# Kernel tuning notes

Hardware: AMD Instinct MI355X
Metric: run time of the kernel (lower is better)

The kernel has to match this reference:

```python
import jax, jax.numpy as jnp
import numpy as np

B, LQ, LK, D = 8, 2048, 2048, 128

def setup_inputs() -> dict:
    key = jax.random.key(0)
    k1, k2, k3, k4 = jax.random.split(key, 4)
    return {
        "query": jax.random.normal(k1, (B, LQ, D), dtype=jnp.float32),
        "key": jax.random.normal(k2, (B, LK, D), dtype=jnp.float32),
        "value": jax.random.normal(k3, (B, LK, D), dtype=jnp.float32),
        "scale_factor": jax.random.normal(k4, (B, LQ, LK), dtype=jnp.float32),
    }

def reference(query, key, value, scale_factor):
    # qk: [B, LQ, LK]
    qk = jnp.einsum("bqd,bkd->bqk", query, key)
    probs = jax.nn.softmax(qk * scale_factor, axis=-1)
    # dropout_p = 0.0 -> identity
    return jnp.einsum("bqk,bkd->bqd", probs, value)
```

## Files before the change

kernel.cpp:

```cpp
#include <hip/hip_runtime.h>
#include <hip/hip_bf16.h>


typedef float          f32x4  __attribute__((ext_vector_type(4)));
typedef float          f32x16 __attribute__((ext_vector_type(16)));
typedef short          s16x8  __attribute__((ext_vector_type(8)));
typedef unsigned int   u32x4  __attribute__((ext_vector_type(4)));
typedef unsigned short u16x4  __attribute__((ext_vector_type(4)));

typedef const __attribute__((address_space(1))) unsigned int* gas_ptr;
typedef __attribute__((address_space(3))) unsigned int*       las_ptr;

#define LOG2E 1.4426950408889634f

__device__ __forceinline__ float fast_exp2(float x) {
#if __has_builtin(__builtin_amdgcn_exp2f)
    return __builtin_amdgcn_exp2f(x);
#else
    return exp2f(x);
#endif
}
__device__ __forceinline__ unsigned short f2bf(float x) {
    return __builtin_bit_cast(unsigned short, __float2bfloat16(x));
}
__device__ __forceinline__ float bf2f(unsigned short u) {
    return __bfloat162float(__builtin_bit_cast(__hip_bfloat16, u));
}

__global__ void conv_split2(const float* __restrict__ q, const float* __restrict__ k,
                            unsigned short* __restrict__ qh, unsigned short* __restrict__ ql,
                            unsigned short* __restrict__ kh, unsigned short* __restrict__ kl) {
    const int bid  = blockIdx.x;
    const int half = bid >> 11;
    const int i    = (bid & 2047) * 256 + threadIdx.x;
    const float* src = half ? k : q;
    unsigned short* hi = half ? kh : qh;
    unsigned short* lo = half ? kl : ql;
    const float4 v = ((const float4*)src)[i];
    float f[4] = {v.x, v.y, v.z, v.w};
    u16x4 h, l;
#pragma unroll
    for (int j = 0; j < 4; ++j) {
        unsigned short hb = f2bf(f[j]);
        h[j] = hb;
        l[j] = f2bf(f[j] - bf2f(hb));
    }
    ((u16x4*)hi)[i] = h;
    ((u16x4*)lo)[i] = l;
}

__global__ void transpose_v(const float* __restrict__ v,
                            unsigned short* __restrict__ vt) {
    __shared__ unsigned short tile[64 * 36];
    const int b    = blockIdx.x & 7;
    const int rest = blockIdx.x >> 3;
    const int k0   = (rest & 31) * 64;
    const int d0   = (rest >> 5) * 32;
    const int tid  = threadIdx.x;
#pragma unroll
    for (int it = 0; it < 2; ++it) {
        int idx = it * 256 + tid;
        int kk  = idx >> 3;
        int d4  = idx & 7;
        float4 val = ((const float4*)v)[((b * 2048 + k0 + kk) * 128 + d0 + d4 * 4) >> 2];
        u16x4 t4;
        t4[0] = f2bf(val.x); t4[1] = f2bf(val.y);
        t4[2] = f2bf(val.z); t4[3] = f2bf(val.w);
        *(u16x4*)&tile[kk * 36 + d4 * 4] = t4;
    }
    __syncthreads();
    {
        int d  = tid >> 3;
        int k8 = tid & 7;
        u16x4 a, cgrp;
#pragma unroll
        for (int j = 0; j < 4; ++j) a[j]    = tile[(k8 * 8 + j) * 36 + d];
#pragma unroll
        for (int j = 0; j < 4; ++j) cgrp[j] = tile[(k8 * 8 + 4 + j) * 36 + d];
        unsigned short* outp = vt + (b * 128 + d0 + d) * 2048 + k0 + k8 * 8;
        *(u16x4*)outp       = a;
        *(u16x4*)(outp + 4) = cgrp;
    }
}

#define NKC 16
#define LDS_TOTAL 79360
#define PBUF_OFF  67584
#define MSTAT_OFF 77824
#define LSTAT_OFF 78848

__global__ __launch_bounds__(256, 2)
void flash_fwd(const unsigned short* __restrict__ qh_g,
               const unsigned short* __restrict__ ql_g,
               const unsigned short* __restrict__ kh_g,
               const unsigned short* __restrict__ kl_g,
               const unsigned short* __restrict__ vt_g,
               const float* __restrict__ scale_g,
               float* __restrict__ out) {
    __shared__ unsigned char smem[LDS_TOTAL];
    unsigned char* khbuf = smem;
    float* mstat = (float*)(smem + MSTAT_OFF);
    float* lstat = (float*)(smem + LSTAT_OFF);
    float* oex   = (float*)smem;

    const int tid  = threadIdx.x;
    const int wave = tid >> 6;
    const int lane = tid & 63;
    const int qi   = lane & 31;
    const int g2   = lane >> 5;

    const int bid = blockIdx.x;
    const int b   = bid & 7;
    const int qt  = bid >> 3;
    const int q0  = qt * 32;
    const int qrow = b * 2048 + q0 + qi;

    unsigned short* pw = (unsigned short*)(smem + PBUF_OFF + wave * 2560);

    s16x8 qhB[8], qlB[8];
#pragma unroll
    for (int s = 0; s < 8; ++s) {
        int idx = qrow * 16 + s * 2 + g2;
        qhB[s] = __builtin_bit_cast(s16x8, ((const u32x4*)qh_g)[idx]);
        qlB[s] = __builtin_bit_cast(s16x8, ((const u32x4*)ql_g)[idx]);
    }

    f32x16 oacc[4];
#pragma unroll
    for (int t = 0; t < 4; ++t)
#pragma unroll
        for (int r = 0; r < 16; ++r) oacc[t][r] = 0.f;
    float m_run = -INFINITY, l_run = 0.f;

    const int krow_base = b * 2048;

    {
#pragma unroll
        for (int j = 0; j < 8; ++j) {
            int o  = wave * 8192 + j * 1024 + lane * 16;
            int r  = o >> 8;
            int cp = (o >> 4) & 15;
            int cn = cp ^ (r & 7);
            const unsigned short* src = kh_g + ((krow_base + r) * 16 + cn) * 8;
            __builtin_amdgcn_global_load_lds((gas_ptr)(const void*)src,
                (las_ptr)(void*)(khbuf + wave * 8192 + j * 1024), 16, 0, 0);
        }
    }
    f32x4 scf[4];
    {
        const int sidx = qrow * 512 + wave * 8 + g2;
#pragma unroll
        for (int rg = 0; rg < 4; ++rg)
            scf[rg] = ((const f32x4*)scale_g)[sidx + rg * 2];
    }
    __syncthreads();

    for (int kc = 0; kc < NKC; ++kc) {
        const int k0  = kc * 128;
        const int cur = kc & 1;
        unsigned char* bufc = khbuf + cur * 32768;

        if (kc + 1 < NKC) {
            unsigned char* bufn = khbuf + (cur ^ 1) * 32768;
#pragma unroll
            for (int j = 0; j < 8; ++j) {
                int o  = wave * 8192 + j * 1024 + lane * 16;
                int r  = o >> 8;
                int cp = (o >> 4) & 15;
                int cn = cp ^ (r & 7);
                const unsigned short* src = kh_g + ((krow_base + k0 + 128 + r) * 16 + cn) * 8;
                __builtin_amdgcn_global_load_lds((gas_ptr)(const void*)src,
                    (las_ptr)(void*)(bufn + wave * 8192 + j * 1024), 16, 0, 0);
            }
        }

        u32x4 klr[8], vr[8];
        {
            const int krow = krow_base + k0 + wave * 32 + qi;
#pragma unroll
            for (int s = 0; s < 8; ++s)
                klr[s] = ((const u32x4*)kl_g)[krow * 16 + s * 2 + g2];
            const int vbase = (b * 128 + qi) * 256 + ((k0 + wave * 32) >> 3) + g2;
#pragma unroll
            for (int t = 0; t < 4; ++t)
#pragma unroll
                for (int s2 = 0; s2 < 2; ++s2)
                    vr[t * 2 + s2] = ((const u32x4*)vt_g)[vbase + t * 32 * 256 + s2 * 2];
        }

        f32x4 scn[4];
        if (kc + 1 < NKC) {
            const int sidx = qrow * 512 + ((k0 + 128) >> 2) + wave * 8 + g2;
#pragma unroll
            for (int rg = 0; rg < 4; ++rg)
                scn[rg] = ((const f32x4*)scale_g)[sidx + rg * 2];
        }

        f32x16 S;
#pragma unroll
        for (int r = 0; r < 16; ++r) S[r] = 0.f;
        s16x8 khf[8];
        {
            const int r  = wave * 32 + qi;
            const int rx = r & 7;
#pragma unroll
            for (int s = 0; s < 8; ++s) {
                int cp = (s * 2 + g2) ^ rx;
                khf[s] = *(const s16x8*)(bufc + r * 256 + cp * 16);
                S = __builtin_amdgcn_mfma_f32_32x32x16_bf16(khf[s], qhB[s], S, 0, 0, 0);
            }
#pragma unroll
            for (int s = 0; s < 8; ++s)
                S = __builtin_amdgcn_mfma_f32_32x32x16_bf16(
                        __builtin_bit_cast(s16x8, klr[s]), qhB[s], S, 0, 0, 0);
#pragma unroll
            for (int s = 0; s < 8; ++s)
                S = __builtin_amdgcn_mfma_f32_32x32x16_bf16(khf[s], qlB[s], S, 0, 0, 0);
        }

        float lt[16];
        float mx = -INFINITY;
#pragma unroll
        for (int r = 0; r < 16; ++r) {
            lt[r] = S[r] * (scf[r >> 2][r & 3] * LOG2E);
            mx = fmaxf(mx, lt[r]);
        }
        mx = fmaxf(mx, __shfl_xor(mx, 32));
        const int par = (kc & 1) * 128;
        if (g2 == 0) mstat[par + wave * 32 + qi] = mx;
        __syncthreads();

        float m_new = m_run;
#pragma unroll
        for (int w = 0; w < 4; ++w)
            m_new = fmaxf(m_new, mstat[par + w * 32 + qi]);
        const float al = fast_exp2(m_run - m_new);
        m_run = m_new;
#pragma unroll
        for (int t = 0; t < 4; ++t)
#pragma unroll
            for (int r = 0; r < 16; ++r) oacc[t][r] *= al;

        float rs = 0.f;
#pragma unroll
        for (int p = 0; p < 8; ++p) {
            float e0 = fast_exp2(lt[2 * p]     - m_new);
            float e1 = fast_exp2(lt[2 * p + 1] - m_new);
            rs += e0 + e1;
            unsigned int pk = (unsigned int)f2bf(e0) | ((unsigned int)f2bf(e1) << 16);
            int kk0 = ((2 * p) & 3) + 8 * (p >> 1) + 4 * g2;
            *(unsigned int*)&pw[qi * 40 + kk0] = pk;
        }
        rs += __shfl_xor(rs, 32);
        l_run = l_run * al + rs;

        s16x8 bP[2];
#pragma unroll
        for (int s2 = 0; s2 < 2; ++s2)
            bP[s2] = *(const s16x8*)&pw[qi * 40 + s2 * 16 + g2 * 8];
#pragma unroll
        for (int t = 0; t < 4; ++t)
#pragma unroll
            for (int s2 = 0; s2 < 2; ++s2)
                oacc[t] = __builtin_amdgcn_mfma_f32_32x32x16_bf16(
                            __builtin_bit_cast(s16x8, vr[t * 2 + s2]), bP[s2], oacc[t], 0, 0, 0);

        if (kc + 1 < NKC) {
#pragma unroll
            for (int rg = 0; rg < 4; ++rg) scf[rg] = scn[rg];
        }
    }

    if (g2 == 0) lstat[wave * 32 + qi] = l_run;
#pragma unroll
    for (int t = 0; t < 4; ++t)
#pragma unroll
        for (int rg = 0; rg < 4; ++rg) {
            f32x4 v4;
#pragma unroll
            for (int j = 0; j < 4; ++j) v4[j] = oacc[t][rg * 4 + j];
            *(f32x4*)&oex[(wave * 32 + qi) * 132 + t * 32 + rg * 8 + g2 * 4] = v4;
        }
    __syncthreads();
    {
        const int q    = tid >> 3;
        const int dblk = tid & 7;
        const float linv = 1.f / (lstat[q] + lstat[32 + q] + lstat[64 + q] + lstat[96 + q]);
#pragma unroll
        for (int j = 0; j < 4; ++j) {
            const int d = dblk * 16 + j * 4;
            f32x4 acc = *(const f32x4*)&oex[q * 132 + d];
#pragma unroll
            for (int w = 1; w < 4; ++w) {
                f32x4 p = *(const f32x4*)&oex[(w * 32 + q) * 132 + d];
                acc[0] += p[0]; acc[1] += p[1]; acc[2] += p[2]; acc[3] += p[3];
            }
            acc[0] *= linv; acc[1] *= linv; acc[2] *= linv; acc[3] *= linv;
            *(f32x4*)&out[(size_t)(b * 2048 + q0 + q) * 128 + d] = acc;
        }
    }
}

extern "C" void kernel_launch(void* const* d_in, const int* in_sizes, int n_in,
                              void* d_out, int out_size, void* d_ws, size_t ws_size,
                              hipStream_t stream) {
    const float* q  = (const float*)d_in[0];
    const float* k  = (const float*)d_in[1];
    const float* v  = (const float*)d_in[2];
    const float* sc = (const float*)d_in[3];
    float* out = (float*)d_out;

    char* ws = (char*)d_ws;
    const size_t MB = 1024 * 1024;
    unsigned short* qh = (unsigned short*)(ws);
    unsigned short* ql = (unsigned short*)(ws + 4 * MB);
    unsigned short* kh = (unsigned short*)(ws + 8 * MB);
    unsigned short* kl = (unsigned short*)(ws + 12 * MB);
    unsigned short* vt = (unsigned short*)(ws + 16 * MB);

    conv_split2<<<4096, 256, 0, stream>>>(q, k, qh, ql, kh, kl);
    transpose_v<<<1024, 256, 0, stream>>>(v, vt);
    flash_fwd<<<512, 256, 0, stream>>>(qh, ql, kh, kl, vt, sc, out);
}
```

Baseline: 299.7 us.

## Rewrite attention with fp16 split, fragment-major layouts, single-wave blocks

Replaces the bf16 hi/lo split with an fp16 split and drops the K low part, cutting the QK^T MFMAs from three passes to two. Q, K and V are prepacked into MFMA-fragment-major layouts by one fused prep kernel, replacing the two earlier prep kernels. The main kernel now runs one wave per 32-query block and streams all 2048 keys, register double-buffering K/V and the scale. This removes the cross-wave max sync and LDS reduction and passes P to the second MFMA through lane shuffles. The trade-offs are fp16 range/precision loss, more K/V reloads per wave, and only 512 single-wave blocks, which may leave the GPU underoccupied.

```diff
diff --git a/kernel.cpp b/kernel.cpp
--- a/kernel.cpp
+++ b/kernel.cpp
@@ -1,15 +1,11 @@
 #include <hip/hip_runtime.h>
-#include <hip/hip_bf16.h>
 
 
 typedef float          f32x4  __attribute__((ext_vector_type(4)));
 typedef float          f32x16 __attribute__((ext_vector_type(16)));
-typedef short          s16x8  __attribute__((ext_vector_type(8)));
+typedef _Float16       h16x8  __attribute__((ext_vector_type(8)));
 typedef unsigned int   u32x4  __attribute__((ext_vector_type(4)));
-typedef unsigned short u16x4  __attribute__((ext_vector_type(4)));
-
-typedef const __attribute__((address_space(1))) unsigned int* gas_ptr;
-typedef __attribute__((address_space(3))) unsigned int*       las_ptr;
+typedef unsigned short u16x8  __attribute__((ext_vector_type(8)));
 
 #define LOG2E 1.4426950408889634f
 
@@ -20,110 +16,110 @@
     return exp2f(x);
 #endif
 }
-__device__ __forceinline__ unsigned short f2bf(float x) {
-    return __builtin_bit_cast(unsigned short, __float2bfloat16(x));
-}
-__device__ __forceinline__ float bf2f(unsigned short u) {
-    return __bfloat162float(__builtin_bit_cast(__hip_bfloat16, u));
-}
-
-__global__ void conv_split2(const float* __restrict__ q, const float* __restrict__ k,
-                            unsigned short* __restrict__ qh, unsigned short* __restrict__ ql,
-                            unsigned short* __restrict__ kh, unsigned short* __restrict__ kl) {
-    const int bid  = blockIdx.x;
-    const int half = bid >> 11;
-    const int i    = (bid & 2047) * 256 + threadIdx.x;
-    const float* src = half ? k : q;
-    unsigned short* hi = half ? kh : qh;
-    unsigned short* lo = half ? kl : ql;
-    const float4 v = ((const float4*)src)[i];
-    float f[4] = {v.x, v.y, v.z, v.w};
-    u16x4 h, l;
-#pragma unroll
-    for (int j = 0; j < 4; ++j) {
-        unsigned short hb = f2bf(f[j]);
-        h[j] = hb;
-        l[j] = f2bf(f[j] - bf2f(hb));
+
+__global__ __launch_bounds__(256)
+void prep_all(const float* __restrict__ q, const float* __restrict__ k,
+              const float* __restrict__ v,
+              unsigned short* __restrict__ qhF, unsigned short* __restrict__ qlF,
+              unsigned short* __restrict__ khF, unsigned short* __restrict__ vF) {
+    const int bid = blockIdx.x;
+    if (bid < 2048) {
+        const bool isQ = bid < 1024;
+        const int t    = (isQ ? bid : bid - 1024) * 256 + threadIdx.x;
+        const int lane = t & 63;
+        const int fr   = t >> 6;
+        const int s    = fr & 7;
+        const int tile = (fr >> 3) & 63;
+        const int b    = fr >> 9;
+        const int row  = b * 2048 + tile * 32 + (lane & 31);
+        const int col  = s * 16 + (lane >> 5) * 8;
+        const float* src = (isQ ? q : k) + row * 128 + col;
+        float f[8];
+        *(f32x4*)&f[0] = *(const f32x4*)src;
+        *(f32x4*)&f[4] = *(const f32x4*)(src + 4);
+        u16x8 hi, lo;
+#pragma unroll
+        for (int j = 0; j < 8; ++j) {
+            _Float16 h = (_Float16)f[j];
+            hi[j] = __builtin_bit_cast(unsigned short, h);
+            _Float16 l = (_Float16)(f[j] - (float)h);
+            lo[j] = __builtin_bit_cast(unsigned short, l);
+        }
+        if (isQ) {
+            *(u16x8*)(qhF + (size_t)t * 8) = hi;
+            *(u16x8*)(qlF + (size_t)t * 8) = lo;
+        } else {
+            *(u16x8*)(khF + (size_t)t * 8) = hi;
+        }
+    } else {
+        __shared__ unsigned short tile[32 * 132];
+        const int id = bid - 2048;
+        const int b  = id >> 6;
+        const int kc = id & 63;
+        const int tid = threadIdx.x;
+#pragma unroll
+        for (int it = 0; it < 4; ++it) {
+            int idx = it * 256 + tid;
+            int kk  = idx >> 5;
+            int c4  = idx & 31;
+            f32x4 val = *(const f32x4*)(v + ((b * 2048 + kc * 32 + kk) * 128 + c4 * 4));
+#pragma unroll
+            for (int j = 0; j < 4; ++j)
+                tile[kk * 132 + c4 * 4 + j] =
+                    __builtin_bit_cast(unsigned short, (_Float16)val[j]);
+        }
+        __syncthreads();
+#pragma unroll
+        for (int e = 0; e < 2; ++e) {
+            int fi   = e * 256 + tid;
+            int lane = fi & 63;
+            int fr2  = fi >> 6;
+            int td   = fr2 >> 1;
+            int s2   = fr2 & 1;
+            u16x8 o;
+#pragma unroll
+            for (int j = 0; j < 8; ++j)
+                o[j] = tile[(s2 * 16 + (lane >> 5) * 8 + j) * 132 + td * 32 + (lane & 31)];
+            *(u16x8*)(vF + ((size_t)((b * 64 + kc) * 8 + fr2) * 64 + lane) * 8) = o;
+        }
     }
-    ((u16x4*)hi)[i] = h;
-    ((u16x4*)lo)[i] = l;
-}
-
-__global__ void transpose_v(const float* __restrict__ v,
-                            unsigned short* __restrict__ vt) {
-    __shared__ unsigned short tile[64 * 36];
-    const int b    = blockIdx.x & 7;
-    const int rest = blockIdx.x >> 3;
-    const int k0   = (rest & 31) * 64;
-    const int d0   = (rest >> 5) * 32;
-    const int tid  = threadIdx.x;
-#pragma unroll
-    for (int it = 0; it < 2; ++it) {
-        int idx = it * 256 + tid;
-        int kk  = idx >> 3;
-        int d4  = idx & 7;
-        float4 val = ((const float4*)v)[((b * 2048 + k0 + kk) * 128 + d0 + d4 * 4) >> 2];
-        u16x4 t4;
-        t4[0] = f2bf(val.x); t4[1] = f2bf(val.y);
-        t4[2] = f2bf(val.z); t4[3] = f2bf(val.w);
-        *(u16x4*)&tile[kk * 36 + d4 * 4] = t4;
-    }
-    __syncthreads();
-    {
-        int d  = tid >> 3;
-        int k8 = tid & 7;
-        u16x4 a, cgrp;
-#pragma unroll
-        for (int j = 0; j < 4; ++j) a[j]    = tile[(k8 * 8 + j) * 36 + d];
-#pragma unroll
-        for (int j = 0; j < 4; ++j) cgrp[j] = tile[(k8 * 8 + 4 + j) * 36 + d];
-        unsigned short* outp = vt + (b * 128 + d0 + d) * 2048 + k0 + k8 * 8;
-        *(u16x4*)outp       = a;
-        *(u16x4*)(outp + 4) = cgrp;
-    }
-}
-
-#define NKC 16
-#define LDS_TOTAL 79360
-#define PBUF_OFF  67584
-#define MSTAT_OFF 77824
-#define LSTAT_OFF 78848
-
-__global__ __launch_bounds__(256, 2)
-void flash_fwd(const unsigned short* __restrict__ qh_g,
-               const unsigned short* __restrict__ ql_g,
-               const unsigned short* __restrict__ kh_g,
-               const unsigned short* __restrict__ kl_g,
-               const unsigned short* __restrict__ vt_g,
+}
+
+__global__ __launch_bounds__(64)
+void flash_fwd(const unsigned short* __restrict__ qhF,
+               const unsigned short* __restrict__ qlF,
+               const unsigned short* __restrict__ khF,
+               const unsigned short* __restrict__ vF,
                const float* __restrict__ scale_g,
                float* __restrict__ out) {
-    __shared__ unsigned char smem[LDS_TOTAL];
-    unsigned char* khbuf = smem;
-    float* mstat = (float*)(smem + MSTAT_OFF);
-    float* lstat = (float*)(smem + LSTAT_OFF);
-    float* oex   = (float*)smem;
-
-    const int tid  = threadIdx.x;
-    const int wave = tid >> 6;
-    const int lane = tid & 63;
-    const int qi   = lane & 31;
-    const int g2   = lane >> 5;
+    __shared__ float scbuf[2][32 * 36];
+
+    const int lane = threadIdx.x;
+    const int q31  = lane & 31;
+    const int h    = lane >> 5;
 
     const int bid = blockIdx.x;
     const int b   = bid & 7;
     const int qt  = bid >> 3;
-    const int q0  = qt * 32;
-    const int qrow = b * 2048 + q0 + qi;
-
-    unsigned short* pw = (unsigned short*)(smem + PBUF_OFF + wave * 2560);
-
-    s16x8 qhB[8], qlB[8];
-#pragma unroll
-    for (int s = 0; s < 8; ++s) {
-        int idx = qrow * 16 + s * 2 + g2;
-        qhB[s] = __builtin_bit_cast(s16x8, ((const u32x4*)qh_g)[idx]);
-        qlB[s] = __builtin_bit_cast(s16x8, ((const u32x4*)ql_g)[idx]);
+
+    h16x8 qh[8], ql[8];
+    {
+        const u32x4* qp = (const u32x4*)qhF + ((size_t)(b * 64 + qt) * 8) * 64 + lane;
+        const u32x4* lp = (const u32x4*)qlF + ((size_t)(b * 64 + qt) * 8) * 64 + lane;
+#pragma unroll
+        for (int s = 0; s < 8; ++s) {
+            qh[s] = __builtin_bit_cast(h16x8, qp[s * 64]);
+            ql[s] = __builtin_bit_cast(h16x8, lp[s * 64]);
+        }
     }
+
+    const u32x4* khp = (const u32x4*)khF + ((size_t)(b * 64) * 8) * 64 + lane;
+    const u32x4* vp  = (const u32x4*)vF  + ((size_t)(b * 64) * 8) * 64 + lane;
+
+    int scrow[4];
+#pragma unroll
+    for (int j = 0; j < 4; ++j)
+        scrow[j] = (b * 2048 + qt * 32 + j * 8 + (lane >> 3)) * 2048 + (lane & 7) * 4;
 
     f32x16 oacc[4];
 #pragma unroll
@@ -132,173 +128,127 @@
         for (int r = 0; r < 16; ++r) oacc[t][r] = 0.f;
     float m_run = -INFINITY, l_run = 0.f;
 
-    const int krow_base = b * 2048;
-
-    {
-#pragma unroll
-        for (int j = 0; j < 8; ++j) {
-            int o  = wave * 8192 + j * 1024 + lane * 16;
-            int r  = o >> 8;
-            int cp = (o >> 4) & 15;
-            int cn = cp ^ (r & 7);
-            const unsigned short* src = kh_g + ((krow_base + r) * 16 + cn) * 8;
-            __builtin_amdgcn_global_load_lds((gas_ptr)(const void*)src,
-                (las_ptr)(void*)(khbuf + wave * 8192 + j * 1024), 16, 0, 0);
+    h16x8 khr[2][8], vr[2][8];
+    f32x4 scv[2][4];
+
+#pragma unroll
+    for (int s = 0; s < 8; ++s) khr[0][s] = __builtin_bit_cast(h16x8, khp[s * 64]);
+#pragma unroll
+    for (int f = 0; f < 8; ++f) vr[0][f]  = __builtin_bit_cast(h16x8, vp[f * 64]);
+#pragma unroll
+    for (int j = 0; j < 4; ++j) scv[0][j] = *(const f32x4*)(scale_g + scrow[j]);
+#pragma unroll
+    for (int j = 0; j < 4; ++j) scv[1][j] = *(const f32x4*)(scale_g + scrow[j] + 32);
+#pragma unroll
+    for (int j = 0; j < 4; ++j)
+        *(f32x4*)&scbuf[0][(j * 8 + (lane >> 3)) * 36 + (lane & 7) * 4] = scv[0][j];
+
+    for (int kc2 = 0; kc2 < 32; ++kc2) {
+#pragma unroll
+        for (int u = 0; u < 2; ++u) {
+            const int kc  = kc2 * 2 + u;
+            const int cur = u, nxt = u ^ 1;
+            const int kn  = (kc + 1) & 63;
+            const int ks2 = (kc + 2) & 63;
+
+#pragma unroll
+            for (int s = 0; s < 8; ++s)
+                khr[nxt][s] = __builtin_bit_cast(h16x8, khp[(kn * 8 + s) * 64]);
+#pragma unroll
+            for (int f = 0; f < 8; ++f)
+                vr[nxt][f]  = __builtin_bit_cast(h16x8, vp[(kn * 8 + f) * 64]);
+
+#pragma unroll
+            for (int j = 0; j < 4; ++j)
+                *(f32x4*)&scbuf[nxt][(j * 8 + (lane >> 3)) * 36 + (lane & 7) * 4] = scv[nxt][j];
+
+#pragma unroll
+            for (int j = 0; j < 4; ++j)
+                scv[cur][j] = *(const f32x4*)(scale_g + scrow[j] + ks2 * 32);
+
+            f32x16 S;
+#pragma unroll
+            for (int r = 0; r < 16; ++r) S[r] = 0.f;
+#pragma unroll
+            for (int s = 0; s < 8; ++s) {
+                S = __builtin_amdgcn_mfma_f32_32x32x16_f16(khr[cur][s], qh[s], S, 0, 0, 0);
+                S = __builtin_amdgcn_mfma_f32_32x32x16_f16(khr[cur][s], ql[s], S, 0, 0, 0);
+            }
+
+            f32x4 scf[4];
+#pragma unroll
+            for (int G = 0; G < 4; ++G)
+                scf[G] = *(const f32x4*)&scbuf[cur][q31 * 36 + (2 * G + h) * 4];
+
+            float lt[16];
+            float mx = -INFINITY;
+#pragma unroll
+            for (int r = 0; r < 16; ++r) {
+                lt[r] = S[r] * scf[r >> 2][r & 3];
+                mx = fmaxf(mx, lt[r]);
+            }
+            mx = fmaxf(mx, __shfl_xor(mx, 32));
+            const float m_new = fmaxf(m_run, mx);
+            const float al = fast_exp2((m_run - m_new) * LOG2E);
+            m_run = m_new;
+            float rs = 0.f;
+            float p[16];
+#pragma unroll
+            for (int r = 0; r < 16; ++r) {
+                p[r] = fast_exp2((lt[r] - m_new) * LOG2E);
+                rs += p[r];
+            }
+            rs += __shfl_xor(rs, 32);
+            l_run = l_run * al + rs;
+#pragma unroll
+            for (int t = 0; t < 4; ++t)
+#pragma unroll
+                for (int r = 0; r < 16; ++r) oacc[t][r] *= al;
+
+            unsigned int pa[4], pb[4];
+#pragma unroll
+            for (int G = 0; G < 4; ++G) {
+                pa[G] = __builtin_bit_cast(unsigned int,
+                         __builtin_amdgcn_cvt_pkrtz(p[4 * G + 0], p[4 * G + 1]));
+                pb[G] = __builtin_bit_cast(unsigned int,
+                         __builtin_amdgcn_cvt_pkrtz(p[4 * G + 2], p[4 * G + 3]));
+            }
+            h16x8 B[2];
+#pragma unroll
+            for (int s2 = 0; s2 < 2; ++s2) {
+                const int Gk = 2 * s2 + h;
+                unsigned int sa = h ? pa[2 * s2] : pa[2 * s2 + 1];
+                unsigned int sb = h ? pb[2 * s2] : pb[2 * s2 + 1];
+                unsigned int xa = (unsigned int)__shfl_xor((int)sa, 32);
+                unsigned int xb = (unsigned int)__shfl_xor((int)sb, 32);
+                u32x4 w;
+                w[0] = h ? xa : pa[Gk];
+                w[1] = h ? xb : pb[Gk];
+                w[2] = h ? pa[Gk] : xa;
+                w[3] = h ? pb[Gk] : xb;
+                B[s2] = __builtin_bit_cast(h16x8, w);
+            }
+
+#pragma unroll
+            for (int t = 0; t < 4; ++t)
+#pragma unroll
+                for (int s2 = 0; s2 < 2; ++s2)
+                    oacc[t] = __builtin_amdgcn_mfma_f32_32x32x16_f16(
+                                vr[cur][t * 2 + s2], B[s2], oacc[t], 0, 0, 0);
         }
     }
-    f32x4 scf[4];
-    {
-        const int sidx = qrow * 512 + wave * 8 + g2;
-#pragma unroll
-        for (int rg = 0; rg < 4; ++rg)
-            scf[rg] = ((const f32x4*)scale_g)[sidx + rg * 2];
-    }
-    __syncthreads();
-
-    for (int kc = 0; kc < NKC; ++kc) {
-        const int k0  = kc * 128;
-        const int cur = kc & 1;
-        unsigned char* bufc = khbuf + cur * 32768;
-
-        if (kc + 1 < NKC) {
-            unsigned char* bufn = khbuf + (cur ^ 1) * 32768;
-#pragma unroll
-            for (int j = 0; j < 8; ++j) {
-                int o  = wave * 8192 + j * 1024 + lane * 16;
-                int r  = o >> 8;
-                int cp = (o >> 4) & 15;
-                int cn = cp ^ (r & 7);
-                const unsigned short* src = kh_g + ((krow_base + k0 + 128 + r) * 16 + cn) * 8;
-                __builtin_amdgcn_global_load_lds((gas_ptr)(const void*)src,
-                    (las_ptr)(void*)(bufn + wave * 8192 + j * 1024), 16, 0, 0);
-            }
-        }
-
-        u32x4 klr[8], vr[8];
-        {
-            const int krow = krow_base + k0 + wave * 32 + qi;
-#pragma unroll
-            for (int s = 0; s < 8; ++s)
-                klr[s] = ((const u32x4*)kl_g)[krow * 16 + s * 2 + g2];
-            const int vbase = (b * 128 + qi) * 256 + ((k0 + wave * 32) >> 3) + g2;
-#pragma unroll
-            for (int t = 0; t < 4; ++t)
-#pragma unroll
-                for (int s2 = 0; s2 < 2; ++s2)
-                    vr[t * 2 + s2] = ((const u32x4*)vt_g)[vbase + t * 32 * 256 + s2 * 2];
-        }
-
-        f32x4 scn[4];
-        if (kc + 1 < NKC) {
-            const int sidx = qrow * 512 + ((k0 + 128) >> 2) + wave * 8 + g2;
-#pragma unroll
-            for (int rg = 0; rg < 4; ++rg)
-                scn[rg] = ((const f32x4*)scale_g)[sidx + rg * 2];
-        }
-
-        f32x16 S;
-#pragma unroll
-        for (int r = 0; r < 16; ++r) S[r] = 0.f;
-        s16x8 khf[8];
-        {
-            const int r  = wave * 32 + qi;
-            const int rx = r & 7;
-#pragma unroll
-            for (int s = 0; s < 8; ++s) {
-                int cp = (s * 2 + g2) ^ rx;
-                khf[s] = *(const s16x8*)(bufc + r * 256 + cp * 16);
-                S = __builtin_amdgcn_mfma_f32_32x32x16_bf16(khf[s], qhB[s], S, 0, 0, 0);
-            }
-#pragma unroll
-            for (int s = 0; s < 8; ++s)
-                S = __builtin_amdgcn_mfma_f32_32x32x16_bf16(
-                        __builtin_bit_cast(s16x8, klr[s]), qhB[s], S, 0, 0, 0);
-#pragma unroll
-            for (int s = 0; s < 8; ++s)
-                S = __builtin_amdgcn_mfma_f32_32x32x16_bf16(khf[s], qlB[s], S, 0, 0, 0);
-        }
-
-        float lt[16];
-        float mx = -INFINITY;
-#pragma unroll
-        for (int r = 0; r < 16; ++r) {
-            lt[r] = S[r] * (scf[r >> 2][r & 3] * LOG2E);
-            mx = fmaxf(mx, lt[r]);
-        }
-        mx = fmaxf(mx, __shfl_xor(mx, 32));
-        const int par = (kc & 1) * 128;
-        if (g2 == 0) mstat[par + wave * 32 + qi] = mx;
-        __syncthreads();
-
-        float m_new = m_run;
-#pragma unroll
-        for (int w = 0; w < 4; ++w)
-            m_new = fmaxf(m_new, mstat[par + w * 32 + qi]);
-        const float al = fast_exp2(m_run - m_new);
-        m_run = m_new;
-#pragma unroll
-        for (int t = 0; t < 4; ++t)
-#pragma unroll
-            for (int r = 0; r < 16; ++r) oacc[t][r] *= al;
-
-        float rs = 0.f;
-#pragma unroll
-        for (int p = 0; p < 8; ++p) {
-            float e0 = fast_exp2(lt[2 * p]     - m_new);
-            float e1 = fast_exp2(lt[2 * p + 1] - m_new);
-            rs += e0 + e1;
-            unsigned int pk = (unsigned int)f2bf(e0) | ((unsigned int)f2bf(e1) << 16);
-            int kk0 = ((2 * p) & 3) + 8 * (p >> 1) + 4 * g2;
-            *(unsigned int*)&pw[qi * 40 + kk0] = pk;
-        }
-        rs += __shfl_xor(rs, 32);
-        l_run = l_run * al + rs;
-
-        s16x8 bP[2];
-#pragma unroll
-        for (int s2 = 0; s2 < 2; ++s2)
-            bP[s2] = *(const s16x8*)&pw[qi * 40 + s2 * 16 + g2 * 8];
-#pragma unroll
-        for (int t = 0; t < 4; ++t)
-#pragma unroll
-            for (int s2 = 0; s2 < 2; ++s2)
-                oacc[t] = __builtin_amdgcn_mfma_f32_32x32x16_bf16(
-                            __builtin_bit_cast(s16x8, vr[t * 2 + s2]), bP[s2], oacc[t], 0, 0, 0);
-
-        if (kc + 1 < NKC) {
-#pragma unroll
-            for (int rg = 0; rg < 4; ++rg) scf[rg] = scn[rg];
-        }
-    }
-
-    if (g2 == 0) lstat[wave * 32 + qi] = l_run;
+
+    const float linv = 1.f / l_run;
+    const size_t orow = (size_t)(b * 2048 + qt * 32 + q31) * 128;
 #pragma unroll
     for (int t = 0; t < 4; ++t)
 #pragma unroll
-        for (int rg = 0; rg < 4; ++rg) {
-            f32x4 v4;
-#pragma unroll
-            for (int j = 0; j < 4; ++j) v4[j] = oacc[t][rg * 4 + j];
-            *(f32x4*)&oex[(wave * 32 + qi) * 132 + t * 32 + rg * 8 + g2 * 4] = v4;
-        }
-    __syncthreads();
-    {
-        const int q    = tid >> 3;
-        const int dblk = tid & 7;
-        const float linv = 1.f / (lstat[q] + lstat[32 + q] + lstat[64 + q] + lstat[96 + q]);
-#pragma unroll
-        for (int j = 0; j < 4; ++j) {
-            const int d = dblk * 16 + j * 4;
-            f32x4 acc = *(const f32x4*)&oex[q * 132 + d];
-#pragma unroll
-            for (int w = 1; w < 4; ++w) {
-                f32x4 p = *(const f32x4*)&oex[(w * 32 + q) * 132 + d];
-                acc[0] += p[0]; acc[1] += p[1]; acc[2] += p[2]; acc[3] += p[3];
-            }
-            acc[0] *= linv; acc[1] *= linv; acc[2] *= linv; acc[3] *= linv;
-            *(f32x4*)&out[(size_t)(b * 2048 + q0 + q) * 128 + d] = acc;
-        }
-    }
+        for (int G = 0; G < 4; ++G) {
+            f32x4 o4;
+#pragma unroll
+            for (int j = 0; j < 4; ++j) o4[j] = oacc[t][4 * G + j] * linv;
+            *(f32x4*)(out + orow + t * 32 + G * 8 + 4 * h) = o4;
+        }
 }
 
 extern "C" void kernel_launch(void* const* d_in, const int* in_sizes, int n_in,
@@ -312,13 +262,11 @@
 
     char* ws = (char*)d_ws;
     const size_t MB = 1024 * 1024;
-    unsigned short* qh = (unsigned short*)(ws);
-    unsigned short* ql = (unsigned short*)(ws + 4 * MB);
-    unsigned short* kh = (unsigned short*)(ws + 8 * MB);
-    unsigned short* kl = (unsigned short*)(ws + 12 * MB);
-    unsigned short* vt = (unsigned short*)(ws + 16 * MB);
-
-    conv_split2<<<4096, 256, 0, stream>>>(q, k, qh, ql, kh, kl);
-    transpose_v<<<1024, 256, 0, stream>>>(v, vt);
-    flash_fwd<<<512, 256, 0, stream>>>(qh, ql, kh, kl, vt, sc, out);
-}
+    unsigned short* qhF = (unsigned short*)(ws);
+    unsigned short* qlF = (unsigned short*)(ws + 4 * MB);
+    unsigned short* khF = (unsigned short*)(ws + 8 * MB);
+    unsigned short* vF  = (unsigned short*)(ws + 12 * MB);
+
+    prep_all<<<2560, 256, 0, stream>>>(q, k, v, qhF, qlF, khF, vF);
+    flash_fwd<<<512, 64, 0, stream>>>(qhF, qlF, khF, vF, sc, out);
+}
```

Measured after the change: 296.7 us. Within noise of the previous version (-1.0%).
